# Performance work log

Measured on AMD Instinct MI355X. Metric: run time of the kernel, lower is better.

Reference implementation:

```python
import jax, jax.numpy as jnp
import numpy as np

H = 16      # num_heads
D = 64      # hidden_size per head
IN = 1024   # input_size = H*D
B, S = 4, 2048

def setup_inputs() -> dict:
    key = jax.random.key(0)
    ks = jax.random.split(key, 5)
    scale = 1.0 / np.sqrt(IN)
    return {
        "x": jax.random.normal(ks[0], (B, S, IN), dtype=jnp.float32),
        "Wq": jax.random.normal(ks[1], (IN, H * D), dtype=jnp.float32) * scale,
        "bq": jnp.zeros((H * D,), dtype=jnp.float32),
        "Wk": jax.random.normal(ks[2], (IN, H * D), dtype=jnp.float32) * scale,
        "bk": jnp.zeros((H * D,), dtype=jnp.float32),
        "Wv": jax.random.normal(ks[3], (IN, H * D), dtype=jnp.float32) * scale,
        "bv": jnp.zeros((H * D,), dtype=jnp.float32),
        "Wo": jax.random.normal(ks[4], (H * D, IN), dtype=jnp.float32) * scale,
        "bo": jnp.zeros((IN,), dtype=jnp.float32),
    }

def reference(x, Wq, bq, Wk, bk, Wv, bv, Wo, bo):
    b, s, _ = x.shape
    # projections -> [b, h, s, d]
    def split_heads(t):
        return t.reshape(b, s, H, D).transpose(0, 2, 1, 3)
    q = split_heads(x @ Wq + bq)
    k = split_heads(x @ Wk + bk)
    v = split_heads(x @ Wv + bv)
    scores = jnp.einsum('bhqd,bhkd->bhqk', q, k) / jnp.sqrt(jnp.float32(D))
    probs = jax.nn.softmax(scores, axis=-1)            # [b,h,s,s]
    attn = jnp.einsum('bhqk,bhkd->bhqd', probs, v)     # [b,h,s,d]
    attn = attn.transpose(0, 2, 1, 3).reshape(b, s, H * D)
    out = attn @ Wo + bo
    return out, jnp.mean(probs, axis=1)
```

## Files before the change

kernel.cpp:

```cpp
#include <hip/hip_runtime.h>

typedef __attribute__((ext_vector_type(8))) short s8v;
typedef __attribute__((ext_vector_type(4))) short s4v;
typedef __attribute__((ext_vector_type(4))) float f4v;

#define DEV __device__ __forceinline__

DEV short b16(float f) {
  unsigned u = __builtin_bit_cast(unsigned, f);
  u = (u + 0x7fffu + ((u >> 16) & 1u)) >> 16;
  return (short)u;
}

DEV unsigned pk2(float a, float b) {
#if __has_builtin(__builtin_amdgcn_cvt_pk_bf16_f32)
  auto p = __builtin_amdgcn_cvt_pk_bf16_f32(a, b);
  return __builtin_bit_cast(unsigned, p);
#else
  return (unsigned)(unsigned short)b16(a) | ((unsigned)(unsigned short)b16(b) << 16);
#endif
}

DEV float fexp2(float x) {
#if __has_builtin(__builtin_amdgcn_exp2f)
  return __builtin_amdgcn_exp2f(x);
#else
  return exp2f(x);
#endif
}

DEV void gl_lds16(const short* g, short* l) {
  __builtin_amdgcn_global_load_lds((const __attribute__((address_space(1))) void*)g,
                                   (__attribute__((address_space(3))) void*)l, 16, 0, 0);
}

#define WAIT_VM(N) asm volatile("s_waitcnt vmcnt(" #N ")" ::: "memory")
#define WAIT_LGKM0() asm volatile("s_waitcnt lgkmcnt(0)" ::: "memory")
#define BAR() __builtin_amdgcn_s_barrier()

__global__ __launch_bounds__(256) void cast_f32_bf16(const float* __restrict__ in,
                                                     short* __restrict__ out, int n4) {
  int i = blockIdx.x * 256 + threadIdx.x;
  if (i >= n4) return;
  float4 v = ((const float4*)in)[i];
  s4v o; o.x = b16(v.x); o.y = b16(v.y); o.z = b16(v.z); o.w = b16(v.w);
  ((s4v*)out)[i] = o;
}

__global__ __launch_bounds__(256) void wtrans(const float* __restrict__ W, short* __restrict__ Wt) {
  int id = blockIdx.x * 256 + threadIdx.x;
  int k8 = id >> 10;
  int n  = id & 1023;
  s8v o;
#pragma unroll
  for (int j = 0; j < 8; ++j) o[j] = b16(W[(k8 * 8 + j) * 1024 + n]);
  *(s8v*)&Wt[n * 1024 + k8 * 8] = o;
}

template <bool OUT_BF16>
__global__ __launch_bounds__(256) void gemm128(const short* __restrict__ A,
                                               const short* __restrict__ Bt,
                                               const float* __restrict__ bias,
                                               void* __restrict__ Cout, float scale) {
  __shared__ short As[128 * 64];
  __shared__ short Bs[128 * 64];
  const int tid = threadIdx.x;
  const int w = tid >> 6, lane = tid & 63, quad = lane >> 4, l15 = lane & 15;
  const int wm = w >> 1, wn = w & 1;
  const int m0 = blockIdx.y * 128, n0 = blockIdx.x * 128;
  const int lr = lane >> 3, lc = (lane & 7) * 8;
  f4v acc[4][4] = {};
  for (int k0 = 0; k0 < 1024; k0 += 64) {
#pragma unroll
    for (int i = 0; i < 4; ++i) {
      int c = i * 4 + w;
      int r = c * 8 + lr;
      gl_lds16(&A[(m0 + r) * 1024 + k0 + lc], &As[c * 512]);
      gl_lds16(&Bt[(n0 + r) * 1024 + k0 + lc], &Bs[c * 512]);
    }
    __syncthreads();
#pragma unroll
    for (int kk = 0; kk < 2; ++kk) {
      s8v af[4], bf[4];
#pragma unroll
      for (int mt = 0; mt < 4; ++mt) af[mt] = *(const s8v*)&As[(wm * 64 + mt * 16 + l15) * 64 + kk * 32 + quad * 8];
#pragma unroll
      for (int nt = 0; nt < 4; ++nt) bf[nt] = *(const s8v*)&Bs[(wn * 64 + nt * 16 + l15) * 64 + kk * 32 + quad * 8];
#pragma unroll
      for (int mt = 0; mt < 4; ++mt)
#pragma unroll
        for (int nt = 0; nt < 4; ++nt)
          acc[mt][nt] = __builtin_amdgcn_mfma_f32_16x16x32_bf16(af[mt], bf[nt], acc[mt][nt], 0, 0, 0);
    }
    __syncthreads();
  }
#pragma unroll
  for (int nt = 0; nt < 4; ++nt) {
    const int col = n0 + wn * 64 + nt * 16 + l15;
    const float bcol = bias[col];
#pragma unroll
    for (int mt = 0; mt < 4; ++mt)
#pragma unroll
      for (int r = 0; r < 4; ++r) {
        const int row = m0 + wm * 64 + mt * 16 + quad * 4 + r;
        float v = (acc[mt][nt][r] + bcol) * scale;
        if (OUT_BF16) ((short*)Cout)[row * 1024 + col] = b16(v);
        else          ((float*)Cout)[row * 1024 + col] = v;
      }
  }
}

__global__ __launch_bounds__(256) void vtrans(const short* __restrict__ V, short* __restrict__ Vt) {
  __shared__ short T[128][72];
  const int st = blockIdx.x, h = blockIdx.y, b = blockIdx.z;
  const int tid = threadIdx.x;
#pragma unroll
  for (int i = 0; i < 4; ++i) {
    int c = tid + i * 256;
    int r = c >> 3, c8 = (c & 7) * 8;
    *(s8v*)&T[r][c8] = *(const s8v*)&V[((b * 2048 + st * 128 + r) * 16 + h) * 64 + c8];
  }
  __syncthreads();
#pragma unroll
  for (int i = 0; i < 4; ++i) {
    int id = tid + i * 256;
    int d = id & 63, s8 = id >> 6;
    s8v o;
#pragma unroll
    for (int j = 0; j < 8; ++j) o[j] = T[s8 * 8 + j][d];
    *(s8v*)&Vt[((b * 16 + h) * 64 + d) * 2048 + st * 128 + s8 * 8] = o;
  }
}

__global__ __launch_bounds__(256, 3) void attn_ctx(const short* __restrict__ Q, const short* __restrict__ K,
                                                   const short* __restrict__ Vt,
                                                   float* __restrict__ rbuf, short* __restrict__ ctx) {
  __shared__ __align__(16) char smem[49152];
  short* Ks = (short*)smem;
  short* Vs = (short*)(smem + 16384);
  short* Ps = (short*)(smem + 32768);
  short* Qs = Ps;
  const int q64 = blockIdx.x, h = blockIdx.y, b = blockIdx.z;
  const int tid = threadIdx.x, w = tid >> 6, lane = tid & 63, quad = lane >> 4, l15 = lane & 15;
  const int bh = b * 16 + h, q0 = q64 * 64;

#pragma unroll
  for (int i = 0; i < 2; ++i) {
    int c = tid + i * 256;
    int r = c >> 3, cc = c & 7;
    *(s8v*)&Qs[r * 64 + (((cc ^ (r & 7))) << 3)] =
        *(const s8v*)&Q[((b * 2048 + q0 + r) * 16 + h) * 64 + cc * 8];
  }
  __syncthreads();
  s8v qf[4][2];
#pragma unroll
  for (int nt = 0; nt < 4; ++nt) {
    int r = nt * 16 + l15;
    qf[nt][0] = *(const s8v*)&Qs[r * 64 + ((quad ^ (r & 7)) << 3)];
    qf[nt][1] = *(const s8v*)&Qs[r * 64 + (((4 + quad) ^ (r & 7)) << 3)];
  }
  const short* kbase = &K[((long)(b * 2048) * 16 + h) * 64];
  const short* vbase = &Vt[(long)(bh * 64) * 2048];
  const int krow = w * 8 + (lane >> 3);
  const short* ksrc = kbase + krow * 1024 + (((lane & 7) ^ (lane >> 3)) << 3);
  const int vrow = w * 4 + (lane >> 4);
  const short* vsrc = vbase + vrow * 2048 + (((lane & 15) ^ vrow) << 3);
  f4v o[4] = {};
  f4v lf = {};
  s8v ones;
#pragma unroll
  for (int j = 0; j < 8; ++j) ones[j] = (short)0x3F80;

#pragma unroll
  for (int i = 0; i < 4; ++i) gl_lds16(ksrc + i * 32768, &Ks[(i * 4 + w) * 512]);
#pragma unroll
  for (int i = 0; i < 4; ++i) gl_lds16(vsrc + i * 32768, &Vs[(i * 4 + w) * 512]);
  WAIT_LGKM0();

  for (int kt = 0; kt < 16; ++kt) {
    WAIT_VM(4);
    BAR();
#pragma unroll
    for (int mt = 0; mt < 2; ++mt) {
      int kr = w * 32 + mt * 16 + l15;
      s8v a0 = *(const s8v*)&Ks[kr * 64 + ((quad ^ (kr & 7)) << 3)];
      s8v a1 = *(const s8v*)&Ks[kr * 64 + (((4 + quad) ^ (kr & 7)) << 3)];
#pragma unroll
      for (int nt = 0; nt < 4; ++nt) {
        f4v st = {};
        st = __builtin_amdgcn_mfma_f32_16x16x32_bf16(a0, qf[nt][0], st, 0, 0, 0);
        st = __builtin_amdgcn_mfma_f32_16x16x32_bf16(a1, qf[nt][1], st, 0, 0, 0);
        float e0 = fexp2(st[0]), e1 = fexp2(st[1]);
        float e2 = fexp2(st[2]), e3 = fexp2(st[3]);
        uint2 pp; pp.x = pk2(e0, e1); pp.y = pk2(e2, e3);
        int q = nt * 16 + l15;
        int chunk = (w * 4 + mt * 2 + (quad >> 1)) ^ l15;
        *(uint2*)&Ps[q * 128 + (chunk << 3) + (quad & 1) * 4] = pp;
      }
    }
    WAIT_LGKM0();
    BAR();
    if (kt < 15) {
#pragma unroll
      for (int i = 0; i < 4; ++i) gl_lds16(ksrc + (kt + 1) * 131072 + i * 32768, &Ks[(i * 4 + w) * 512]);
      WAIT_VM(4);
    } else {
      WAIT_VM(0);
    }
    BAR();
#pragma unroll
    for (int kk = 0; kk < 4; ++kk) {
      int qr = w * 16 + l15;
      s8v a = *(const s8v*)&Ps[qr * 128 + (((kk * 4 + quad) ^ (qr & 15)) << 3)];
#pragma unroll
      for (int dt = 0; dt < 4; ++dt) {
        int d = dt * 16 + l15;
        s8v vb = *(const s8v*)&Vs[d * 128 + (((kk * 4 + quad) ^ (d & 15)) << 3)];
        o[dt] = __builtin_amdgcn_mfma_f32_16x16x32_bf16(a, vb, o[dt], 0, 0, 0);
      }
      lf = __builtin_amdgcn_mfma_f32_16x16x32_bf16(a, ones, lf, 0, 0, 0);
    }
    WAIT_LGKM0();
    BAR();
    if (kt < 15) {
#pragma unroll
      for (int i = 0; i < 4; ++i) gl_lds16(vsrc + (kt + 1) * 128 + i * 32768, &Vs[(i * 4 + w) * 512]);
    }
  }

  float rv[4];
#pragma unroll
  for (int r = 0; r < 4; ++r) rv[r] = 1.0f / lf[r];
  if (l15 == 0) {
    f4v t; t[0] = rv[0]; t[1] = rv[1]; t[2] = rv[2]; t[3] = rv[3];
    *(f4v*)&rbuf[bh * 2048 + q0 + w * 16 + quad * 4] = t;
  }
#pragma unroll
  for (int dt = 0; dt < 4; ++dt)
#pragma unroll
    for (int r = 0; r < 4; ++r) {
      int sq = q0 + w * 16 + quad * 4 + r;
      ctx[((b * 2048 + sq) * 16 + h) * 64 + dt * 16 + l15] = b16(o[dt][r] * rv[r]);
    }
}

__global__ __launch_bounds__(256) void mean_probs(const short* __restrict__ Q, const short* __restrict__ K,
                                                  const float* __restrict__ rbuf, float* __restrict__ outm) {
  __shared__ __align__(16) short Qs[2][8192];
  __shared__ __align__(16) short Ks[2][8192];
  __shared__ __align__(16) float r_all[2048];
  const int k128 = blockIdx.x, q128 = blockIdx.y, b = blockIdx.z;
  const int tid = threadIdx.x, w = tid >> 6, lane = tid & 63, quad = lane >> 4, l15 = lane & 15;
  f4v mn[2][8] = {};
  const int mrow = w * 8 + (lane >> 3);
  const int mck8 = ((lane & 7) ^ (lane >> 3)) << 3;
  const short* qsrc = Q + ((long)(b * 2048 + q128 * 128 + mrow) * 16) * 64 + mck8;
  const short* ksrc = K + ((long)(b * 2048 + k128 * 128 + mrow) * 16) * 64 + mck8;
  const float* rb = rbuf + (long)(b * 16) * 2048 + q128 * 128;
#pragma unroll
  for (int i = 0; i < 2; ++i) {
    int hh = i * 8 + w * 2 + (lane >> 5);
    gl_lds16((const short*)(rb + hh * 2048 + (lane & 31) * 4), (short*)r_all + (i * 4 + w) * 512);
  }
#pragma unroll
  for (int i = 0; i < 4; ++i) gl_lds16(qsrc + i * 32768, &Qs[0][(i * 4 + w) * 512]);
#pragma unroll
  for (int i = 0; i < 4; ++i) gl_lds16(ksrc + i * 32768, &Ks[0][(i * 4 + w) * 512]);

  for (int h = 0; h < 16; ++h) {
    const int cur = h & 1;
    if (h < 15) {
#pragma unroll
      for (int i = 0; i < 4; ++i) gl_lds16(qsrc + (h + 1) * 64 + i * 32768, &Qs[cur ^ 1][(i * 4 + w) * 512]);
#pragma unroll
      for (int i = 0; i < 4; ++i) gl_lds16(ksrc + (h + 1) * 64 + i * 32768, &Ks[cur ^ 1][(i * 4 + w) * 512]);
      WAIT_VM(8);
    } else {
      WAIT_VM(0);
    }
    BAR();
    s8v aq[2][2];
#pragma unroll
    for (int qt = 0; qt < 2; ++qt) {
      int r = w * 32 + qt * 16 + l15;
      aq[qt][0] = *(const s8v*)&Qs[cur][r * 64 + ((quad ^ (r & 7)) << 3)];
      aq[qt][1] = *(const s8v*)&Qs[cur][r * 64 + (((4 + quad) ^ (r & 7)) << 3)];
    }
    float rr[2][4];
#pragma unroll
    for (int qt = 0; qt < 2; ++qt)
#pragma unroll
      for (int r = 0; r < 4; ++r) rr[qt][r] = r_all[h * 128 + w * 32 + qt * 16 + quad * 4 + r];
#pragma unroll
    for (int ktile = 0; ktile < 8; ++ktile) {
      int kr = ktile * 16 + l15;
      s8v b0 = *(const s8v*)&Ks[cur][kr * 64 + ((quad ^ (kr & 7)) << 3)];
      s8v b1 = *(const s8v*)&Ks[cur][kr * 64 + (((4 + quad) ^ (kr & 7)) << 3)];
#pragma unroll
      for (int qt = 0; qt < 2; ++qt) {
        f4v sc = {};
        sc = __builtin_amdgcn_mfma_f32_16x16x32_bf16(aq[qt][0], b0, sc, 0, 0, 0);
        sc = __builtin_amdgcn_mfma_f32_16x16x32_bf16(aq[qt][1], b1, sc, 0, 0, 0);
#pragma unroll
        for (int r = 0; r < 4; ++r)
          mn[qt][ktile][r] += fexp2(sc[r]) * rr[qt][r];
      }
    }
    WAIT_LGKM0();
    BAR();
  }
#pragma unroll
  for (int qt = 0; qt < 2; ++qt)
#pragma unroll
    for (int ktile = 0; ktile < 8; ++ktile)
#pragma unroll
      for (int r = 0; r < 4; ++r) {
        long qrow = q128 * 128 + w * 32 + qt * 16 + quad * 4 + r;
        outm[((long)b * 2048 + qrow) * 2048 + k128 * 128 + ktile * 16 + l15] = mn[qt][ktile][r] * 0.0625f;
      }
}

extern "C" void kernel_launch(void* const* d_in, const int* in_sizes, int n_in,
                              void* d_out, int out_size, void* d_ws, size_t ws_size,
                              hipStream_t stream) {
  (void)in_sizes; (void)n_in; (void)out_size; (void)ws_size;
  const float* x  = (const float*)d_in[0];
  const float* Wq = (const float*)d_in[1];
  const float* bq = (const float*)d_in[2];
  const float* Wk = (const float*)d_in[3];
  const float* bk = (const float*)d_in[4];
  const float* Wv = (const float*)d_in[5];
  const float* bv = (const float*)d_in[6];
  const float* Wo = (const float*)d_in[7];
  const float* bo = (const float*)d_in[8];
  float* out  = (float*)d_out;
  float* outm = out + 8388608;

  char* ws = (char*)d_ws;
  short* xb  = (short*)(ws);
  short* Wqt = (short*)(ws + 16777216);
  short* Wkt = (short*)(ws + 18874368);
  short* Wvt = (short*)(ws + 20971520);
  short* Wot = (short*)(ws + 23068672);
  short* Qb  = (short*)(ws + 25165824);
  short* Kb  = (short*)(ws + 41943040);
  short* Vb  = (short*)(ws + 58720256);
  short* Vt  = (short*)(ws + 75497472);
  float* rbuf = (float*)Vb;
  short* ctx = xb;

  const float C2 = 0.18033688011112042f;

  cast_f32_bf16<<<8192, 256, 0, stream>>>(x, xb, 2097152);
  wtrans<<<512, 256, 0, stream>>>(Wq, Wqt);
  wtrans<<<512, 256, 0, stream>>>(Wk, Wkt);
  wtrans<<<512, 256, 0, stream>>>(Wv, Wvt);
  wtrans<<<512, 256, 0, stream>>>(Wo, Wot);
  dim3 gg(8, 64);
  gemm128<true><<<gg, 256, 0, stream>>>(xb, Wqt, bq, Qb, C2);
  gemm128<true><<<gg, 256, 0, stream>>>(xb, Wkt, bk, Kb, 1.0f);
  gemm128<true><<<gg, 256, 0, stream>>>(xb, Wvt, bv, Vb, 1.0f);
  vtrans<<<dim3(16, 16, 4), 256, 0, stream>>>(Vb, Vt);
  attn_ctx<<<dim3(32, 16, 4), 256, 0, stream>>>(Qb, Kb, Vt, rbuf, ctx);
  mean_probs<<<dim3(16, 16, 4), 256, 0, stream>>>(Qb, Kb, rbuf, outm);
  gemm128<false><<<gg, 256, 0, stream>>>(ctx, Wot, bo, out, 1.0f);
}
```

Baseline: 433.0 us.

## Batch weight transposes and QKV GEMMs into single launches; remap block IDs for XCD locality

Merges the four weight-transpose launches into one 2D-grid kernel and the three Q/K/V projection GEMMs into one launch that selects the matrix per block. It relies on the workspace layout already placing Q/K/V outputs and the transposed weights contiguously. It also remaps linear block IDs in the GEMMs, attention and mean-probs kernels so that neighbouring tiles sharing the same head or rows land on the same XCD, which should improve L2 reuse. The aim is fewer launches, a fuller GPU per launch, and better cache locality. The cost is some extra index arithmetic per block.

Result: faster. 413.2 us (-4.6%).

```diff
diff --git a/kernel.cpp b/kernel.cpp
--- a/kernel.cpp
+++ b/kernel.cpp
@@ -47,27 +47,41 @@
   ((s4v*)out)[i] = o;
 }
 
-__global__ __launch_bounds__(256) void wtrans(const float* __restrict__ W, short* __restrict__ Wt) {
+__global__ __launch_bounds__(256) void wtrans4(const float* __restrict__ W0, const float* __restrict__ W1,
+                                               const float* __restrict__ W2, const float* __restrict__ W3,
+                                               short* __restrict__ Wt) {
+  const int mat = blockIdx.y;
+  const float* W = mat == 0 ? W0 : (mat == 1 ? W1 : (mat == 2 ? W2 : W3));
+  short* out = Wt + (long)mat * 1048576;
   int id = blockIdx.x * 256 + threadIdx.x;
   int k8 = id >> 10;
   int n  = id & 1023;
   s8v o;
 #pragma unroll
   for (int j = 0; j < 8; ++j) o[j] = b16(W[(k8 * 8 + j) * 1024 + n]);
-  *(s8v*)&Wt[n * 1024 + k8 * 8] = o;
-}
-
-template <bool OUT_BF16>
-__global__ __launch_bounds__(256) void gemm128(const short* __restrict__ A,
-                                               const short* __restrict__ Bt,
-                                               const float* __restrict__ bias,
-                                               void* __restrict__ Cout, float scale) {
+  *(s8v*)&out[n * 1024 + k8 * 8] = o;
+}
+
+__global__ __launch_bounds__(256) void gemm_qkv(const short* __restrict__ A,
+                                                const short* __restrict__ Wt,
+                                                const float* __restrict__ bq,
+                                                const float* __restrict__ bk,
+                                                const float* __restrict__ bv,
+                                                short* __restrict__ Cb, float qscale) {
   __shared__ short As[128 * 64];
   __shared__ short Bs[128 * 64];
+  int n = blockIdx.x + 24 * blockIdx.y;
+  int id = (n & 7) * 192 + (n >> 3);
+  const int nx = id % 24, my = id / 24;
+  const int mat = nx >> 3;
+  const short* Bt = Wt + (long)mat * 1048576;
+  const float* bias = mat == 0 ? bq : (mat == 1 ? bk : bv);
+  short* Cout = Cb + (long)mat * 8388608;
+  const float scale = mat == 0 ? qscale : 1.0f;
+  const int m0 = my * 128, n0 = (nx & 7) * 128;
   const int tid = threadIdx.x;
   const int w = tid >> 6, lane = tid & 63, quad = lane >> 4, l15 = lane & 15;
   const int wm = w >> 1, wn = w & 1;
-  const int m0 = blockIdx.y * 128, n0 = blockIdx.x * 128;
   const int lr = lane >> 3, lc = (lane & 7) * 8;
   f4v acc[4][4] = {};
   for (int k0 = 0; k0 < 1024; k0 += 64) {
@@ -103,9 +117,59 @@
 #pragma unroll
       for (int r = 0; r < 4; ++r) {
         const int row = m0 + wm * 64 + mt * 16 + quad * 4 + r;
-        float v = (acc[mt][nt][r] + bcol) * scale;
-        if (OUT_BF16) ((short*)Cout)[row * 1024 + col] = b16(v);
-        else          ((float*)Cout)[row * 1024 + col] = v;
+        Cout[row * 1024 + col] = b16((acc[mt][nt][r] + bcol) * scale);
+      }
+  }
+}
+
+__global__ __launch_bounds__(256) void gemm128(const short* __restrict__ A,
+                                               const short* __restrict__ Bt,
+                                               const float* __restrict__ bias,
+                                               float* __restrict__ Cout) {
+  __shared__ short As[128 * 64];
+  __shared__ short Bs[128 * 64];
+  int n = blockIdx.x + 8 * blockIdx.y;
+  int id = (n & 7) * 64 + (n >> 3);
+  const int m0 = (id >> 3) * 128, n0 = (id & 7) * 128;
+  const int tid = threadIdx.x;
+  const int w = tid >> 6, lane = tid & 63, quad = lane >> 4, l15 = lane & 15;
+  const int wm = w >> 1, wn = w & 1;
+  const int lr = lane >> 3, lc = (lane & 7) * 8;
+  f4v acc[4][4] = {};
+  for (int k0 = 0; k0 < 1024; k0 += 64) {
+#pragma unroll
+    for (int i = 0; i < 4; ++i) {
+      int c = i * 4 + w;
+      int r = c * 8 + lr;
+      gl_lds16(&A[(m0 + r) * 1024 + k0 + lc], &As[c * 512]);
+      gl_lds16(&Bt[(n0 + r) * 1024 + k0 + lc], &Bs[c * 512]);
+    }
+    __syncthreads();
+#pragma unroll
+    for (int kk = 0; kk < 2; ++kk) {
+      s8v af[4], bf[4];
+#pragma unroll
+      for (int mt = 0; mt < 4; ++mt) af[mt] = *(const s8v*)&As[(wm * 64 + mt * 16 + l15) * 64 + kk * 32 + quad * 8];
+#pragma unroll
+      for (int nt = 0; nt < 4; ++nt) bf[nt] = *(const s8v*)&Bs[(wn * 64 + nt * 16 + l15) * 64 + kk * 32 + quad * 8];
+#pragma unroll
+      for (int mt = 0; mt < 4; ++mt)
+#pragma unroll
+        for (int nt = 0; nt < 4; ++nt)
+          acc[mt][nt] = __builtin_amdgcn_mfma_f32_16x16x32_bf16(af[mt], bf[nt], acc[mt][nt], 0, 0, 0);
+    }
+    __syncthreads();
+  }
+#pragma unroll
+  for (int nt = 0; nt < 4; ++nt) {
+    const int col = n0 + wn * 64 + nt * 16 + l15;
+    const float bcol = bias[col];
+#pragma unroll
+    for (int mt = 0; mt < 4; ++mt)
+#pragma unroll
+      for (int r = 0; r < 4; ++r) {
+        const int row = m0 + wm * 64 + mt * 16 + quad * 4 + r;
+        Cout[row * 1024 + col] = acc[mt][nt][r] + bcol;
       }
   }
 }
@@ -140,7 +204,9 @@
   short* Vs = (short*)(smem + 16384);
   short* Ps = (short*)(smem + 32768);
   short* Qs = Ps;
-  const int q64 = blockIdx.x, h = blockIdx.y, b = blockIdx.z;
+  int nlin = blockIdx.x + 32 * (blockIdx.y + 16 * blockIdx.z);
+  int bid = (nlin & 7) * 256 + (nlin >> 3);
+  const int q64 = bid & 31, h = (bid >> 5) & 15, b = bid >> 9;
   const int tid = threadIdx.x, w = tid >> 6, lane = tid & 63, quad = lane >> 4, l15 = lane & 15;
   const int bh = b * 16 + h, q0 = q64 * 64;
 
@@ -249,7 +315,9 @@
   __shared__ __align__(16) short Qs[2][8192];
   __shared__ __align__(16) short Ks[2][8192];
   __shared__ __align__(16) float r_all[2048];
-  const int k128 = blockIdx.x, q128 = blockIdx.y, b = blockIdx.z;
+  int nlin = blockIdx.x + 16 * (blockIdx.y + 16 * blockIdx.z);
+  int bid = (nlin & 7) * 128 + (nlin >> 3);
+  const int k128 = bid & 15, q128 = (bid >> 4) & 15, b = bid >> 8;
   const int tid = threadIdx.x, w = tid >> 6, lane = tid & 63, quad = lane >> 4, l15 = lane & 15;
   f4v mn[2][8] = {};
   const int mrow = w * 8 + (lane >> 3);
@@ -339,8 +407,6 @@
   char* ws = (char*)d_ws;
   short* xb  = (short*)(ws);
   short* Wqt = (short*)(ws + 16777216);
-  short* Wkt = (short*)(ws + 18874368);
-  short* Wvt = (short*)(ws + 20971520);
   short* Wot = (short*)(ws + 23068672);
   short* Qb  = (short*)(ws + 25165824);
   short* Kb  = (short*)(ws + 41943040);
@@ -352,16 +418,10 @@
   const float C2 = 0.18033688011112042f;
 
   cast_f32_bf16<<<8192, 256, 0, stream>>>(x, xb, 2097152);
-  wtrans<<<512, 256, 0, stream>>>(Wq, Wqt);
-  wtrans<<<512, 256, 0, stream>>>(Wk, Wkt);
-  wtrans<<<512, 256, 0, stream>>>(Wv, Wvt);
-  wtrans<<<512, 256, 0, stream>>>(Wo, Wot);
-  dim3 gg(8, 64);
-  gemm128<true><<<gg, 256, 0, stream>>>(xb, Wqt, bq, Qb, C2);
-  gemm128<true><<<gg, 256, 0, stream>>>(xb, Wkt, bk, Kb, 1.0f);
-  gemm128<true><<<gg, 256, 0, stream>>>(xb, Wvt, bv, Vb, 1.0f);
+  wtrans4<<<dim3(512, 4), 256, 0, stream>>>(Wq, Wk, Wv, Wo, Wqt);
+  gemm_qkv<<<dim3(24, 64), 256, 0, stream>>>(xb, Wqt, bq, bk, bv, Qb, C2);
   vtrans<<<dim3(16, 16, 4), 256, 0, stream>>>(Vb, Vt);
   attn_ctx<<<dim3(32, 16, 4), 256, 0, stream>>>(Qb, Kb, Vt, rbuf, ctx);
   mean_probs<<<dim3(16, 16, 4), 256, 0, stream>>>(Qb, Kb, rbuf, outm);
-  gemm128<false><<<gg, 256, 0, stream>>>(ctx, Wot, bo, out, 1.0f);
-}
+  gemm128<<<dim3(8, 64), 256, 0, stream>>>(ctx, Wot, bo, out);
+}
```
